# Optimization experiments

Measured on AMD Instinct MI355X. Metric: run time of the kernel, lower is better.

Reference implementation:

```python
import jax, jax.numpy as jnp
import numpy as np

B, T, D_IN, H, D_OUT = 4096, 512, 8, 50, 1

def setup_inputs() -> dict:
    key = jax.random.key(0)
    ks = jax.random.split(key, 7)
    s_ih = 1.0 / np.sqrt(H)
    return {
        "x": jax.random.normal(ks[0], (B, T, D_IN), dtype=jnp.float32),
        # torch nn.RNN params: weight_ih_l0 [H, D_IN], weight_hh_l0 [H, H], biases [H]
        "W_ih": jax.random.uniform(ks[1], (H, D_IN), minval=-s_ih, maxval=s_ih, dtype=jnp.float32),
        "W_hh": jax.random.uniform(ks[2], (H, H), minval=-s_ih, maxval=s_ih, dtype=jnp.float32),
        "b_ih": jax.random.uniform(ks[3], (H,), minval=-s_ih, maxval=s_ih, dtype=jnp.float32),
        "b_hh": jax.random.uniform(ks[4], (H,), minval=-s_ih, maxval=s_ih, dtype=jnp.float32),
        # fc: Linear(H, D_OUT)
        "fc_W": jax.random.uniform(ks[5], (D_OUT, H), minval=-s_ih, maxval=s_ih, dtype=jnp.float32),
        "fc_b": jax.random.uniform(ks[6], (D_OUT,), minval=-s_ih, maxval=s_ih, dtype=jnp.float32),
    }

def reference(x, W_ih, W_hh, b_ih, b_hh, fc_W, fc_b):
    # Vanilla RNN: h_t = tanh(x_t @ W_ih^T + b_ih + h_{t-1} @ W_hh^T + b_hh)
    # Precompute input projections for all timesteps (one big GEMM),
    # then scan the recurrence over time. Only the last hidden state is
    # needed because the module reads out[:, -1, :].
    xW = jnp.einsum('btd,hd->bth', x, W_ih) + (b_ih + b_hh)  # [B, T, H]
    xW_t = jnp.swapaxes(xW, 0, 1)  # [T, B, H] for scan over time

    def step(h, xw_t):
        h_new = jnp.tanh(xw_t + h @ W_hh.T)
        return h_new, None

    h0 = jnp.zeros((x.shape[0], W_hh.shape[0]), dtype=x.dtype)
    h_last, _ = jax.lax.scan(step, h0, xW_t)
    # fc on last timestep hidden
    return h_last @ fc_W.T + fc_b  # [B, D_OUT]
```

## Files before the change

### kernel.cpp

```cpp
#include <hip/hip_runtime.h>

#define B_TOT 4096
#define T_LEN 512
#define DIN   8
#define H_DIM 50
#define BPB   8

typedef __attribute__((ext_vector_type(8))) short  short8;
typedef __attribute__((ext_vector_type(4))) float  floatx4;

__device__ __forceinline__ ushort f2bf_rne(float f) {
  uint u = __float_as_uint(f);
  u += 0x7FFFu + ((u >> 16) & 1u);
  return (ushort)(u >> 16);
}
__device__ __forceinline__ ushort f2bf_trunc(float f) {
  return (ushort)(__float_as_uint(f) >> 16);
}
__device__ __forceinline__ float bf2f(ushort b) {
  return __uint_as_float(((uint)b) << 16);
}
__device__ __forceinline__ float fast_tanh(float v) {
  float e = __expf(2.0f * v);
  return 1.0f - 2.0f * __builtin_amdgcn_rcpf(1.0f + e);
}

#define ROWS 72
#define REG  1152

__global__ __launch_bounds__(256) void rnn_fused(
    const float* __restrict__ x, const float* __restrict__ W_ih,
    const float* __restrict__ W_hh, const float* __restrict__ b_ih,
    const float* __restrict__ b_hh, const float* __restrict__ fc_W,
    const float* __restrict__ fc_b, float* __restrict__ out)
{
  __shared__ __align__(16) ushort lds[4 * REG];

  const int tid  = threadIdx.x;
  const int lane = tid & 63;
  const int wave = tid >> 6;
  const int col  = lane & 15;
  const int kg   = lane >> 4;
  const int b0   = blockIdx.x * BPB;

  const int iGlob = wave * 16 + col;
  union U8 { ushort u[8]; short8 v; };
  U8 Bh0u, Bh1u, Bl0u, Bl1u;
#pragma unroll
  for (int hf = 0; hf < 2; ++hf) {
#pragma unroll
    for (int j = 0; j < 8; ++j) {
      int k = hf * 32 + kg * 8 + j;
      float w = 0.f;
      if (iGlob < H_DIM) {
        if (k < H_DIM)            w = W_hh[iGlob * H_DIM + k];
        else if (k < H_DIM + DIN) w = W_ih[iGlob * DIN + (k - H_DIM)];
      }
      ushort hi = f2bf_rne(w);
      ushort lo = f2bf_trunc(w - bf2f(hi));
      if (hf == 0) { Bh0u.u[j] = hi; Bl0u.u[j] = lo; }
      else         { Bh1u.u[j] = hi; Bl1u.u[j] = lo; }
    }
  }
  const short8 Bh0 = Bh0u.v, Bh1 = Bh1u.v, Bl0 = Bl0u.v, Bl1 = Bl1u.v;

  const float bv = (iGlob < H_DIM) ? (b_ih[iGlob] + b_hh[iGlob]) : 0.f;
  const floatx4 biasf = {bv, bv, bv, bv};

  for (int z = tid; z < 4 * REG; z += 256) lds[z] = 0;
  __syncthreads();

  const int xm = lane >> 3;
  const int xd = lane & 7;
  const float* xp = x + ((size_t)(b0 + xm) * T_LEN) * DIN + xd;
  float px1 = 0.f, px2 = 0.f, px3 = 0.f;
  if (wave == 3) {
    float x0 = xp[0];
    ushort xh = f2bf_trunc(x0);
    lds[0 * REG + xm * ROWS + H_DIM + xd] = xh;
    lds[1 * REG + xm * ROWS + H_DIM + xd] = f2bf_trunc(x0 - bf2f(xh));
    px1 = xp[8]; px2 = xp[16]; px3 = xp[24];
  }
  __syncthreads();

  const bool epi = (iGlob < H_DIM) && (kg < 2);

  auto step = [&](int t, int offph, int offpl, int offqh, int offql) {
    const int rb = col * ROWS + kg * 8;
    short8 Ah0 = *(const short8*)(lds + offph + rb);
    short8 Ah1 = *(const short8*)(lds + offph + rb + 32);
    short8 Al0 = *(const short8*)(lds + offpl + rb);
    short8 Al1 = *(const short8*)(lds + offpl + rb + 32);

    floatx4 accA = biasf;
    accA = __builtin_amdgcn_mfma_f32_16x16x32_bf16(Ah0, Bh0, accA, 0, 0, 0);
    accA = __builtin_amdgcn_mfma_f32_16x16x32_bf16(Ah1, Bh1, accA, 0, 0, 0);
    floatx4 accB = {0.f, 0.f, 0.f, 0.f};
    accB = __builtin_amdgcn_mfma_f32_16x16x32_bf16(Ah0, Bl0, accB, 0, 0, 0);
    accB = __builtin_amdgcn_mfma_f32_16x16x32_bf16(Ah1, Bl1, accB, 0, 0, 0);
    floatx4 accC = {0.f, 0.f, 0.f, 0.f};
    accC = __builtin_amdgcn_mfma_f32_16x16x32_bf16(Al0, Bh0, accC, 0, 0, 0);
    accC = __builtin_amdgcn_mfma_f32_16x16x32_bf16(Al1, Bh1, accC, 0, 0, 0);

    if (epi) {
#pragma unroll
      for (int r = 0; r < 4; ++r) {
        float v  = accA[r] + accB[r] + accC[r];
        float th = fast_tanh(v);
        uint  u  = __float_as_uint(th);
        float hf2 = __uint_as_float(u & 0xFFFF0000u);
        float lf  = th - hf2;
        int m = kg * 4 + r;
        lds[offqh + m * ROWS + iGlob] = (ushort)(u >> 16);
        lds[offql + m * ROWS + iGlob] = f2bf_trunc(lf);
      }
    }
    if (wave == 3) {
      ushort xh = f2bf_trunc(px1);
      ushort xl = f2bf_trunc(px1 - bf2f(xh));
      lds[offqh + xm * ROWS + H_DIM + xd] = xh;
      lds[offql + xm * ROWS + H_DIM + xd] = xl;
      px1 = px2; px2 = px3;
      int tn = t + 4; if (tn > T_LEN - 1) tn = T_LEN - 1;
      px3 = xp[tn * DIN];
    }
    __syncthreads();
  };

  for (int t = 0; t < T_LEN; t += 2) {
    step(t,     0 * REG, 1 * REG, 2 * REG, 3 * REG);
    step(t + 1, 2 * REG, 3 * REG, 0 * REG, 1 * REG);
  }

  if (tid < BPB * 4) {
    int m = tid >> 2, kq = tid & 3;
    float acc2 = 0.f;
    for (int k = kq; k < H_DIM; k += 4) {
      float hv = bf2f(lds[0 * REG + m * ROWS + k]) + bf2f(lds[1 * REG + m * ROWS + k]);
      acc2 += hv * fc_W[k];
    }
    acc2 += __shfl_xor(acc2, 1);
    acc2 += __shfl_xor(acc2, 2);
    if (kq == 0) out[b0 + m] = acc2 + fc_b[0];
  }
}

extern "C" void kernel_launch(void* const* d_in, const int* in_sizes, int n_in,
                              void* d_out, int out_size, void* d_ws, size_t ws_size,
                              hipStream_t stream) {
  const float* x    = (const float*)d_in[0];
  const float* W_ih = (const float*)d_in[1];
  const float* W_hh = (const float*)d_in[2];
  const float* b_ih = (const float*)d_in[3];
  const float* b_hh = (const float*)d_in[4];
  const float* fc_W = (const float*)d_in[5];
  const float* fc_b = (const float*)d_in[6];
  rnn_fused<<<dim3(B_TOT / BPB), dim3(256), 0, stream>>>(
      x, W_ih, W_hh, b_ih, b_hh, fc_W, fc_b, (float*)d_out);
}
```

Before: 321.0 us.

## Run each RNN block as a single wave with 16 batch rows and no barriers

Replaces the 4-wave, 8-row block with one 64-lane wave that handles 16 batch rows and all four 16-wide hidden tiles, holding every split-bf16 weight fragment in registers. Within a single wave, the per-timestep __syncthreads is replaced by a plain LDS wait, which removes barrier cost from the serial recurrence. It also swaps the MFMA operand roles so the hidden state becomes the B operand, and packs the LDS writes. The trade-off is twice the serial MFMA and tanh work per wave per step, plus higher register use, in exchange for losing the cross-wave sync and halving the block count.

```diff
diff --git a/kernel.cpp b/kernel.cpp
--- a/kernel.cpp
+++ b/kernel.cpp
@@ -4,7 +4,7 @@
 #define T_LEN 512
 #define DIN   8
 #define H_DIM 50
-#define BPB   8
+#define BPB   16
 
 typedef __attribute__((ext_vector_type(8))) short  short8;
 typedef __attribute__((ext_vector_type(4))) float  floatx4;
@@ -20,15 +20,21 @@
 __device__ __forceinline__ float bf2f(ushort b) {
   return __uint_as_float(((uint)b) << 16);
 }
-__device__ __forceinline__ float fast_tanh(float v) {
-  float e = __expf(2.0f * v);
-  return 1.0f - 2.0f * __builtin_amdgcn_rcpf(1.0f + e);
+#define WAIT() asm volatile("s_waitcnt lgkmcnt(0)" ::: "memory")
+
+__device__ __forceinline__ void tanh_split(float v, ushort& h, ushort& l) {
+  float e  = __expf(2.0f * v);
+  float th = 1.0f - 2.0f * __builtin_amdgcn_rcpf(1.0f + e);
+  uint  u  = __float_as_uint(th);
+  h = (ushort)(u >> 16);
+  float hf = __uint_as_float(u & 0xFFFF0000u);
+  l = f2bf_trunc(th - hf);
 }
 
 #define ROWS 72
 #define REG  1152
 
-__global__ __launch_bounds__(256) void rnn_fused(
+__global__ __launch_bounds__(64) void rnn_1wave(
     const float* __restrict__ x, const float* __restrict__ W_ih,
     const float* __restrict__ W_hh, const float* __restrict__ b_ih,
     const float* __restrict__ b_hh, const float* __restrict__ fc_W,
@@ -36,112 +42,133 @@
 {
   __shared__ __align__(16) ushort lds[4 * REG];
 
-  const int tid  = threadIdx.x;
-  const int lane = tid & 63;
-  const int wave = tid >> 6;
+  const int lane = threadIdx.x;
   const int col  = lane & 15;
   const int kg   = lane >> 4;
   const int b0   = blockIdx.x * BPB;
 
-  const int iGlob = wave * 16 + col;
   union U8 { ushort u[8]; short8 v; };
-  U8 Bh0u, Bh1u, Bl0u, Bl1u;
+  short8 Wh[4][2], Wl[4][2];
 #pragma unroll
-  for (int hf = 0; hf < 2; ++hf) {
+  for (int t4 = 0; t4 < 4; ++t4) {
+    const int iG = t4 * 16 + col;
 #pragma unroll
-    for (int j = 0; j < 8; ++j) {
-      int k = hf * 32 + kg * 8 + j;
-      float w = 0.f;
-      if (iGlob < H_DIM) {
-        if (k < H_DIM)            w = W_hh[iGlob * H_DIM + k];
-        else if (k < H_DIM + DIN) w = W_ih[iGlob * DIN + (k - H_DIM)];
+    for (int kh = 0; kh < 2; ++kh) {
+      U8 hi_u, lo_u;
+#pragma unroll
+      for (int j = 0; j < 8; ++j) {
+        int k = kh * 32 + kg * 8 + j;
+        float w = 0.f;
+        if (iG < H_DIM) {
+          if (k < H_DIM)            w = W_hh[iG * H_DIM + k];
+          else if (k < H_DIM + DIN) w = W_ih[iG * DIN + (k - H_DIM)];
+        }
+        ushort h = f2bf_rne(w);
+        hi_u.u[j] = h;
+        lo_u.u[j] = f2bf_trunc(w - bf2f(h));
       }
-      ushort hi = f2bf_rne(w);
-      ushort lo = f2bf_trunc(w - bf2f(hi));
-      if (hf == 0) { Bh0u.u[j] = hi; Bl0u.u[j] = lo; }
-      else         { Bh1u.u[j] = hi; Bl1u.u[j] = lo; }
+      Wh[t4][kh] = hi_u.v;
+      Wl[t4][kh] = lo_u.v;
     }
   }
-  const short8 Bh0 = Bh0u.v, Bh1 = Bh1u.v, Bl0 = Bl0u.v, Bl1 = Bl1u.v;
 
-  const float bv = (iGlob < H_DIM) ? (b_ih[iGlob] + b_hh[iGlob]) : 0.f;
-  const floatx4 biasf = {bv, bv, bv, bv};
+  floatx4 bias[4];
+#pragma unroll
+  for (int t4 = 0; t4 < 4; ++t4)
+#pragma unroll
+    for (int r = 0; r < 4; ++r) {
+      int iG = t4 * 16 + kg * 4 + r;
+      bias[t4][r] = (iG < H_DIM) ? (b_ih[iG] + b_hh[iG]) : 0.f;
+    }
 
-  for (int z = tid; z < 4 * REG; z += 256) lds[z] = 0;
-  __syncthreads();
+  for (int z = lane; z < 2304; z += 64) ((uint*)lds)[z] = 0;
+  WAIT();
 
-  const int xm = lane >> 3;
-  const int xd = lane & 7;
-  const float* xp = x + ((size_t)(b0 + xm) * T_LEN) * DIN + xd;
-  float px1 = 0.f, px2 = 0.f, px3 = 0.f;
-  if (wave == 3) {
-    float x0 = xp[0];
-    ushort xh = f2bf_trunc(x0);
-    lds[0 * REG + xm * ROWS + H_DIM + xd] = xh;
-    lds[1 * REG + xm * ROWS + H_DIM + xd] = f2bf_trunc(x0 - bf2f(xh));
-    px1 = xp[8]; px2 = xp[16]; px3 = xp[24];
+  const float2* xp2 = (const float2*)(x + ((size_t)(b0 + col) * T_LEN) * DIN) + kg;
+  {
+    float2 x0 = xp2[0];
+    ushort h0x = f2bf_trunc(x0.x), h0y = f2bf_trunc(x0.y);
+    *(uint*)&lds[0 * REG + col * ROWS + H_DIM + 2 * kg] = (uint)h0x | ((uint)h0y << 16);
+    uint lx = (uint)f2bf_trunc(x0.x - bf2f(h0x)) | ((uint)f2bf_trunc(x0.y - bf2f(h0y)) << 16);
+    *(uint*)&lds[1 * REG + col * ROWS + H_DIM + 2 * kg] = lx;
   }
-  __syncthreads();
+  float2 px1 = xp2[4], px2 = xp2[8], px3 = xp2[12];
+  int toff = 16;
+  WAIT();
 
-  const bool epi = (iGlob < H_DIM) && (kg < 2);
+  const int rdoff = col * ROWS + kg * 8;
+  const int wroff = col * ROWS;
 
-  auto step = [&](int t, int offph, int offpl, int offqh, int offql) {
-    const int rb = col * ROWS + kg * 8;
-    short8 Ah0 = *(const short8*)(lds + offph + rb);
-    short8 Ah1 = *(const short8*)(lds + offph + rb + 32);
-    short8 Al0 = *(const short8*)(lds + offpl + rb);
-    short8 Al1 = *(const short8*)(lds + offpl + rb + 32);
+  auto step = [&](int pr, int qr) {
+    const ushort* rp = lds + pr + rdoff;
+    short8 Bh0 = *(const short8*)(rp);
+    short8 Bh1 = *(const short8*)(rp + 32);
+    short8 Bl0 = *(const short8*)(rp + REG);
+    short8 Bl1 = *(const short8*)(rp + REG + 32);
 
-    floatx4 accA = biasf;
-    accA = __builtin_amdgcn_mfma_f32_16x16x32_bf16(Ah0, Bh0, accA, 0, 0, 0);
-    accA = __builtin_amdgcn_mfma_f32_16x16x32_bf16(Ah1, Bh1, accA, 0, 0, 0);
-    floatx4 accB = {0.f, 0.f, 0.f, 0.f};
-    accB = __builtin_amdgcn_mfma_f32_16x16x32_bf16(Ah0, Bl0, accB, 0, 0, 0);
-    accB = __builtin_amdgcn_mfma_f32_16x16x32_bf16(Ah1, Bl1, accB, 0, 0, 0);
-    floatx4 accC = {0.f, 0.f, 0.f, 0.f};
-    accC = __builtin_amdgcn_mfma_f32_16x16x32_bf16(Al0, Bh0, accC, 0, 0, 0);
-    accC = __builtin_amdgcn_mfma_f32_16x16x32_bf16(Al1, Bh1, accC, 0, 0, 0);
+    floatx4 v[4];
+#pragma unroll
+    for (int t4 = 0; t4 < 4; ++t4) {
+      floatx4 a = bias[t4];
+      a = __builtin_amdgcn_mfma_f32_16x16x32_bf16(Wh[t4][0], Bh0, a, 0, 0, 0);
+      a = __builtin_amdgcn_mfma_f32_16x16x32_bf16(Wh[t4][1], Bh1, a, 0, 0, 0);
+      floatx4 b = {0.f, 0.f, 0.f, 0.f};
+      b = __builtin_amdgcn_mfma_f32_16x16x32_bf16(Wl[t4][0], Bh0, b, 0, 0, 0);
+      b = __builtin_amdgcn_mfma_f32_16x16x32_bf16(Wl[t4][1], Bh1, b, 0, 0, 0);
+      floatx4 c = {0.f, 0.f, 0.f, 0.f};
+      c = __builtin_amdgcn_mfma_f32_16x16x32_bf16(Wh[t4][0], Bl0, c, 0, 0, 0);
+      c = __builtin_amdgcn_mfma_f32_16x16x32_bf16(Wh[t4][1], Bl1, c, 0, 0, 0);
+#pragma unroll
+      for (int r = 0; r < 4; ++r) v[t4][r] = a[r] + b[r] + c[r];
+    }
 
-    if (epi) {
+    ushort* wp = lds + qr + wroff;
 #pragma unroll
-      for (int r = 0; r < 4; ++r) {
-        float v  = accA[r] + accB[r] + accC[r];
-        float th = fast_tanh(v);
-        uint  u  = __float_as_uint(th);
-        float hf2 = __uint_as_float(u & 0xFFFF0000u);
-        float lf  = th - hf2;
-        int m = kg * 4 + r;
-        lds[offqh + m * ROWS + iGlob] = (ushort)(u >> 16);
-        lds[offql + m * ROWS + iGlob] = f2bf_trunc(lf);
-      }
+    for (int t4 = 0; t4 < 3; ++t4) {
+      ushort h0, h1, h2, h3, l0, l1, l2, l3;
+      tanh_split(v[t4][0], h0, l0);
+      tanh_split(v[t4][1], h1, l1);
+      tanh_split(v[t4][2], h2, l2);
+      tanh_split(v[t4][3], h3, l3);
+      uint2 hv = { (uint)h0 | ((uint)h1 << 16), (uint)h2 | ((uint)h3 << 16) };
+      uint2 lv = { (uint)l0 | ((uint)l1 << 16), (uint)l2 | ((uint)l3 << 16) };
+      *(uint2*)(wp + t4 * 16 + kg * 4)       = hv;
+      *(uint2*)(wp + REG + t4 * 16 + kg * 4) = lv;
     }
-    if (wave == 3) {
-      ushort xh = f2bf_trunc(px1);
-      ushort xl = f2bf_trunc(px1 - bf2f(xh));
-      lds[offqh + xm * ROWS + H_DIM + xd] = xh;
-      lds[offql + xm * ROWS + H_DIM + xd] = xl;
+    if (kg == 0) {
+      ushort h0, h1, l0, l1;
+      tanh_split(v[3][0], h0, l0);
+      tanh_split(v[3][1], h1, l1);
+      *(uint*)(wp + 48)       = (uint)h0 | ((uint)h1 << 16);
+      *(uint*)(wp + REG + 48) = (uint)l0 | ((uint)l1 << 16);
+    }
+    {
+      ushort hx = f2bf_trunc(px1.x), hy = f2bf_trunc(px1.y);
+      *(uint*)(wp + H_DIM + 2 * kg) = (uint)hx | ((uint)hy << 16);
+      uint lx = (uint)f2bf_trunc(px1.x - bf2f(hx)) | ((uint)f2bf_trunc(px1.y - bf2f(hy)) << 16);
+      *(uint*)(wp + REG + H_DIM + 2 * kg) = lx;
       px1 = px2; px2 = px3;
-      int tn = t + 4; if (tn > T_LEN - 1) tn = T_LEN - 1;
-      px3 = xp[tn * DIN];
+      px3 = xp2[toff];
+      toff += 4; if (toff > (T_LEN - 1) * 4) toff = (T_LEN - 1) * 4;
     }
-    __syncthreads();
+    WAIT();
   };
 
   for (int t = 0; t < T_LEN; t += 2) {
-    step(t,     0 * REG, 1 * REG, 2 * REG, 3 * REG);
-    step(t + 1, 2 * REG, 3 * REG, 0 * REG, 1 * REG);
+    step(0, 2 * REG);
+    step(2 * REG, 0);
   }
 
-  if (tid < BPB * 4) {
-    int m = tid >> 2, kq = tid & 3;
-    float acc2 = 0.f;
+  {
+    int m = lane >> 2, kq = lane & 3;
+    float acc = 0.f;
     for (int k = kq; k < H_DIM; k += 4) {
-      float hv = bf2f(lds[0 * REG + m * ROWS + k]) + bf2f(lds[1 * REG + m * ROWS + k]);
-      acc2 += hv * fc_W[k];
+      float hv = bf2f(lds[m * ROWS + k]) + bf2f(lds[REG + m * ROWS + k]);
+      acc += hv * fc_W[k];
     }
-    acc2 += __shfl_xor(acc2, 1);
-    acc2 += __shfl_xor(acc2, 2);
-    if (kq == 0) out[b0 + m] = acc2 + fc_b[0];
+    acc += __shfl_xor(acc, 1);
+    acc += __shfl_xor(acc, 2);
+    if (kq == 0) out[b0 + m] = acc + fc_b[0];
   }
 }
 
@@ -155,6 +182,6 @@
   const float* b_hh = (const float*)d_in[4];
   const float* fc_W = (const float*)d_in[5];
   const float* fc_b = (const float*)d_in[6];
-  rnn_fused<<<dim3(B_TOT / BPB), dim3(256), 0, stream>>>(
+  rnn_1wave<<<dim3(B_TOT / BPB), dim3(64), 0, stream>>>(
       x, W_ih, W_hh, b_ih, b_hh, fc_W, fc_b, (float*)d_out);
 }
```

Measured after the change: 441.8 us. 1.38x slower.
